# Kernel optimization log

Measured on AMD Instinct MI355X. Metric: run time of the kernel, lower is better.

Reference implementation:

```python
import jax, jax.numpy as jnp
import numpy as np

EPS = 1e-6
SIGMA = 1.0       # get_matrix default sigma
INIT_SIGMA = 1.0  # args.init_sigma


def setup_inputs() -> dict:
    key = jax.random.key(0)
    ks = jax.random.split(key, 12)
    B, T, LD, NB = 16, 2048, 256, 32
    s = 1.0 / np.sqrt(LD)
    E_raw = jax.random.normal(ks[5], (LD, LD), jnp.float32)
    E_w, _ = jnp.linalg.qr(E_raw)  # orthogonal like geotorch.orthogonal
    return {
        "Z": jax.random.normal(ks[0], (B, T, LD), jnp.float32),
        "obs_times": jax.random.uniform(ks[1], (B, T, 1), jnp.float32),
        "D": jax.random.normal(ks[2], (NB, LD), jnp.float32),
        "coeff_W": jax.random.normal(ks[3], (NB, LD), jnp.float32) * s,
        "coeff_b": jnp.zeros((NB,), jnp.float32),
        "E_w": E_w.astype(jnp.float32),
        "B_w": jax.random.normal(ks[6], (LD, LD), jnp.float32) * s,
        "C_w": jax.random.normal(ks[7], (LD, LD), jnp.float32) * s,
        "M_w": jax.random.normal(ks[8], (LD, LD), jnp.float32) * s,
        "init_mean_p": jax.random.normal(ks[9], (LD,), jnp.float32),
        "init_log_var": jax.random.normal(ks[10], (LD,), jnp.float32),
        "y_log_var": jax.random.normal(ks[11], (LD,), jnp.float32),
    }


def _binop(qi, qj):
    # (A_j*A_i, Bu_j + A_j*Bu_i): combine earlier element qi with later qj
    A_i, Bu_i = qi
    A_j, Bu_j = qj
    return (A_j * A_i, Bu_j + A_j * Bu_i)


def reference(Z, obs_times, D, coeff_W, coeff_b, E_w, B_w, C_w, M_w,
              init_mean_p, init_log_var, y_log_var):
    LD = Z.shape[-1]
    # alphas = B(Z)
    alphas = jnp.einsum('btd,ed->bte', Z, B_w)                      # (B,T,LD)
    # get_matrix (vectorized over batch and time)
    A_basis = -(jnp.exp(D) + EPS)                                   # (NB,LD), negative
    A_coeff = jax.nn.softmax(jnp.einsum('btd,nd->btn', alphas, coeff_W) + coeff_b, axis=-1)
    A_mat = jnp.einsum('btn,nd->btd', A_coeff, A_basis)             # (B,T,LD)
    exp_A_m = jnp.exp(A_mat * obs_times)                            # mean transition
    exp_B_m = (exp_A_m - 1.0) / A_mat * alphas
    exp_A_v = jnp.exp(2.0 * A_mat * obs_times)                      # var transition
    exp_B_v = 0.5 * SIGMA ** 2 * (exp_A_v - 1.0) / A_mat + EPS
    mats_A = jnp.concatenate([exp_A_m, exp_A_v], axis=-1)           # (B,T,2LD)
    mats_B = jnp.concatenate([exp_B_m, exp_B_v], axis=-1)           # (B,T,2LD)
    # parallel linear-recurrence scan over time
    cum_A, cum_B = jax.lax.associative_scan(_binop, (mats_A, mats_B), axis=1)
    # initial condition in rotated coordinates
    init_mean0 = E_w.T @ init_mean_p                                # (LD,)
    diag_v = INIT_SIGMA * (jnp.exp(init_log_var) + EPS)
    init_var0 = jnp.einsum('ki,k->i', E_w ** 2, diag_v)             # diag(E^T diag(v) E)
    init_mv = jnp.concatenate([init_mean0, init_var0], axis=0)      # (2LD,)
    imv = cum_A * init_mv                                           # (B,T,2LD)
    init_mean, init_var = imv[..., :LD], imv[..., LD:]
    xs_mean, xs_var = cum_B[..., :LD], cum_B[..., LD:]
    y_var = jnp.exp(y_log_var) + EPS
    # output projections: M(E(.)) and history C(E(Z))
    history = jnp.einsum('btd,ed,fe->btf', Z, E_w, C_w)
    means = jnp.einsum('btd,ed,fe->btf', xs_mean + init_mean, E_w, M_w) + history
    stds = jnp.einsum('btd,ed,fe->btf', jnp.sqrt(xs_var + init_var + y_var), E_w, M_w)
    return means, stds, alphas
```

## Files before the change

kernel.cpp:

```cpp
#include <hip/hip_runtime.h>
#include <math.h>

#define EPS 1e-6f

#define B_   16
#define T_   2048
#define LD   256
#define NB   32
#define BT   (B_ * T_)
#define NCH  64
#define CHUNK (T_ / NCH)

typedef short bf16x8 __attribute__((ext_vector_type(8)));
typedef float f32x4  __attribute__((ext_vector_type(4)));

__device__ __forceinline__ unsigned short f2b(float f) {
    unsigned int u = __float_as_uint(f);
    unsigned int r = (u + 0x7fffu + ((u >> 16) & 1u)) >> 16;
    return (unsigned short)r;
}

__device__ __forceinline__ float b2f(unsigned short h) {
    return __uint_as_float(((unsigned int)h) << 16);
}

__device__ __forceinline__ void gl_lds16(const void* g, void* l) {
    __builtin_amdgcn_global_load_lds(
        (const __attribute__((address_space(1))) unsigned int*)g,
        (__attribute__((address_space(3))) unsigned int*)l, 16, 0, 0);
}

__device__ __forceinline__ void stage_tile(const unsigned short* __restrict__ src,
                                           int row0, int stride, int kb,
                                           unsigned short* lds, int wv, int lane) {
#pragma unroll
    for (int cc = 0; cc < 2; ++cc) {
        int c = wv * 2 + cc;
        int r = c * 16 + (lane >> 2);
        int qd = (lane & 3) ^ ((r >> 1) & 3);
        const unsigned short* g = src + (size_t)(row0 + r) * stride + kb + qd * 8;
        gl_lds16(g, lds + c * 512);
    }
}

__device__ __forceinline__ bf16x8 frag_ld(const unsigned short* lds, int row, int qd) {
    int pq = qd ^ ((row >> 1) & 3);
    return *(const bf16x8*)(lds + row * 32 + pq * 8);
}

__device__ __forceinline__ int u_idx(int i, int d) {
    return ((d >> 5) << 10) + (i << 5) + (((((d >> 3) & 3)) ^ (i & 3)) << 3) + (d & 7);
}

__device__ __forceinline__ void compute_Am(const float* __restrict__ logits,
                                           const float* __restrict__ obs,
                                           const unsigned short* __restrict__ AbTh,
                                           const unsigned short* __restrict__ AbTl,
                                           int bt0,
                                           unsigned int* U,
                                           unsigned short* Ph, unsigned short* Pl,
                                           float* obs_s) {
    int tid = threadIdx.x;
    int l = tid & 31, rg = tid >> 5;
    if (tid < CHUNK) obs_s[tid] = obs[bt0 + tid];
#pragma unroll
    for (int jj = 0; jj < 4; ++jj) {
        int row = rg * 4 + jj;
        float v = logits[(size_t)(bt0 + row) * NB + l];
        float mx = v;
#pragma unroll
        for (int off = 16; off >= 1; off >>= 1) mx = fmaxf(mx, __shfl_xor(mx, off, 32));
        float e = expf(v - mx);
        float s = e;
#pragma unroll
        for (int off = 16; off >= 1; off >>= 1) s += __shfl_xor(s, off, 32);
        float p = e / s;
        unsigned short h = f2b(p);
        int sa = row * 32 + ((((l >> 3) ^ ((row >> 1) & 3))) << 3) + (l & 7);
        Ph[sa] = h;
        Pl[sa] = f2b(p - b2f(h));
    }
    __syncthreads();

    int lane = tid & 63, wv = tid >> 6;
    int qd = lane >> 4, mr = lane & 15;
    bf16x8 ph[2], pl[2];
#pragma unroll
    for (int iT = 0; iT < 2; ++iT) {
        ph[iT] = frag_ld(Ph, iT * 16 + mr, qd);
        pl[iT] = frag_ld(Pl, iT * 16 + mr, qd);
    }
#pragma unroll
    for (int j = 0; j < 4; ++j) {
        int dcol = wv * 64 + j * 16 + mr;
        bf16x8 ah = *(const bf16x8*)(AbTh + dcol * NB + qd * 8);
        bf16x8 al = *(const bf16x8*)(AbTl + dcol * NB + qd * 8);
#pragma unroll
        for (int iT = 0; iT < 2; ++iT) {
            f32x4 acc = (f32x4){0.f, 0.f, 0.f, 0.f};
            acc = __builtin_amdgcn_mfma_f32_16x16x32_bf16(ph[iT], ah, acc, 0, 0, 0);
            acc = __builtin_amdgcn_mfma_f32_16x16x32_bf16(pl[iT], ah, acc, 0, 0, 0);
            acc = __builtin_amdgcn_mfma_f32_16x16x32_bf16(ph[iT], al, acc, 0, 0, 0);
#pragma unroll
            for (int r = 0; r < 4; ++r) {
                int i = iT * 16 + qd * 4 + r;
                U[u_idx(i, dcol)] = __float_as_uint(acc[r]);
            }
        }
    }
    __syncthreads();
}

__global__ __launch_bounds__(256) void k_pre(const float* __restrict__ Z,
                                             const float* __restrict__ Dm,
                                             const float* __restrict__ cw,
                                             const float* __restrict__ Ew,
                                             const float* __restrict__ Bw,
                                             const float* __restrict__ Cw,
                                             const float* __restrict__ Mw,
                                             const float* __restrict__ imp,
                                             const float* __restrict__ ilv,
                                             const float* __restrict__ ylv,
                                             unsigned short* __restrict__ GMh,
                                             unsigned short* __restrict__ GCh,
                                             unsigned short* __restrict__ cwbh,
                                             float* __restrict__ im0,
                                             float* __restrict__ iv0,
                                             float* __restrict__ yv,
                                             unsigned short* __restrict__ AbTh,
                                             unsigned short* __restrict__ AbTl,
                                             unsigned short* __restrict__ Bwh,
                                             unsigned short* __restrict__ Zh) {
    int bid = blockIdx.x;
    int tid = threadIdx.x;
    if (bid < 544) {
        const float* W; const float* E; unsigned short* out; int d0, f0;
        if (bid < 256)      { W = Mw; E = Ew; out = GMh;  d0 = (bid & 15) * 16; f0 = (bid >> 4) * 16; }
        else if (bid < 512) { W = Cw; E = Ew; out = GCh;  d0 = (bid & 15) * 16; f0 = ((bid - 256) >> 4) * 16; }
        else                { W = cw; E = Bw; out = cwbh; d0 = (bid & 15) * 16; f0 = ((bid - 512) >> 4) * 16; }
        __shared__ float Ws[16][17];
        __shared__ float Es[16][17];
        int tx = tid & 15, ty = tid >> 4;
        float acc = 0.f;
        for (int eb = 0; eb < LD; eb += 16) {
            Ws[ty][tx] = W[(f0 + ty) * LD + eb + tx];
            Es[ty][tx] = E[(eb + ty) * LD + d0 + tx];
            __syncthreads();
#pragma unroll
            for (int k = 0; k < 16; ++k) acc = fmaf(Ws[ty][k], Es[k][tx], acc);
            __syncthreads();
        }
        out[(f0 + ty) * LD + d0 + tx] = f2b(acc);
    } else if (bid < 577) {
        int sub = bid - 544;
        int t = tid;
        if (sub == 0) {
            float sm = 0.f, sv = 0.f;
            for (int k = 0; k < LD; ++k) {
                float e = Ew[k * LD + t];
                sm = fmaf(e, imp[k], sm);
                sv = fmaf(e * e, expf(ilv[k]) + EPS, sv);
            }
            im0[t] = sm;
            iv0[t] = sv;
            yv[t]  = expf(ylv[t]) + EPS;
        } else {
            int n = sub - 1;
            float a = -(expf(Dm[n * LD + t]) + EPS);
            unsigned short h = f2b(a);
            AbTh[t * NB + n] = h;
            AbTl[t * NB + n] = f2b(a - b2f(h));
        }
    } else if (bid < 641) {
        int i = (bid - 577) * 256 + tid;
        float4 v = ((const float4*)Bw)[i];
        ((ushort4*)Bwh)[i] = make_ushort4(f2b(v.x), f2b(v.y), f2b(v.z), f2b(v.w));
    } else {
        int i = (bid - 641) * 256 + tid;
        float4 v = ((const float4*)Z)[i];
        ((ushort4*)Zh)[i] = make_ushort4(f2b(v.x), f2b(v.y), f2b(v.z), f2b(v.w));
    }
}

__global__ __launch_bounds__(256) void k_zb(const unsigned short* __restrict__ Zh,
                                            const unsigned short* __restrict__ Bwh,
                                            const unsigned short* __restrict__ cwbh,
                                            const float* __restrict__ cb,
                                            float* __restrict__ alphas,
                                            float* __restrict__ logits) {
    __shared__ unsigned short As[128 * 32];
    __shared__ unsigned short Bs[128 * 32];
    int tid = threadIdx.x, lane = tid & 63, wv = tid >> 6;
    int m0 = blockIdx.x * 128;
    int y  = blockIdx.y;
    if (y < 2) {
        int n0 = y * 128;
        int wm = (wv & 1) * 64, wn = (wv >> 1) * 64;
        f32x4 acc[4][4];
#pragma unroll
        for (int i = 0; i < 4; ++i)
#pragma unroll
            for (int j = 0; j < 4; ++j) acc[i][j] = (f32x4){0.f, 0.f, 0.f, 0.f};
        for (int kb = 0; kb < LD; kb += 32) {
            stage_tile(Zh, m0, LD, kb, As, wv, lane);
            stage_tile(Bwh, n0, LD, kb, Bs, wv, lane);
            __syncthreads();
            int qd = lane >> 4;
            bf16x8 af[4], bf[4];
#pragma unroll
            for (int i = 0; i < 4; ++i) af[i] = frag_ld(As, wm + i * 16 + (lane & 15), qd);
#pragma unroll
            for (int j = 0; j < 4; ++j) bf[j] = frag_ld(Bs, wn + j * 16 + (lane & 15), qd);
#pragma unroll
            for (int i = 0; i < 4; ++i)
#pragma unroll
                for (int j = 0; j < 4; ++j)
                    acc[i][j] = __builtin_amdgcn_mfma_f32_16x16x32_bf16(af[i], bf[j], acc[i][j], 0, 0, 0);
            __syncthreads();
        }
        int col = wn + (lane & 15);
        int rb  = wm + ((lane >> 4) << 2);
#pragma unroll
        for (int i = 0; i < 4; ++i)
#pragma unroll
            for (int j = 0; j < 4; ++j)
#pragma unroll
                for (int r = 0; r < 4; ++r)
                    alphas[(size_t)(m0 + rb + i * 16 + r) * LD + n0 + col + j * 16] = acc[i][j][r];
    } else {
        f32x4 acc[2][2];
#pragma unroll
        for (int i = 0; i < 2; ++i)
#pragma unroll
            for (int j = 0; j < 2; ++j) acc[i][j] = (f32x4){0.f, 0.f, 0.f, 0.f};
        for (int kb = 0; kb < LD; kb += 32) {
            stage_tile(Zh, m0, LD, kb, As, wv, lane);
            if (wv < 2) {
                int r = wv * 16 + (lane >> 2);
                int qd = (lane & 3) ^ ((r >> 1) & 3);
                gl_lds16(cwbh + (size_t)r * LD + kb + qd * 8, Bs + wv * 512);
            }
            __syncthreads();
            int qd = lane >> 4;
            bf16x8 af[2], bff[2];
#pragma unroll
            for (int i = 0; i < 2; ++i) af[i] = frag_ld(As, wv * 32 + i * 16 + (lane & 15), qd);
#pragma unroll
            for (int j = 0; j < 2; ++j) bff[j] = frag_ld(Bs, j * 16 + (lane & 15), qd);
#pragma unroll
            for (int i = 0; i < 2; ++i)
#pragma unroll
                for (int j = 0; j < 2; ++j)
                    acc[i][j] = __builtin_amdgcn_mfma_f32_16x16x32_bf16(af[i], bff[j], acc[i][j], 0, 0, 0);
            __syncthreads();
        }
        int col = lane & 15;
        int rb  = (lane >> 4) << 2;
#pragma unroll
        for (int i = 0; i < 2; ++i)
#pragma unroll
            for (int j = 0; j < 2; ++j)
#pragma unroll
                for (int r = 0; r < 4; ++r) {
                    int row = m0 + wv * 32 + i * 16 + rb + r;
                    int cc  = j * 16 + col;
                    logits[(size_t)row * NB + cc] = acc[i][j][r] + cb[cc];
                }
    }
}

__global__ __launch_bounds__(256) void k_tot(const float* __restrict__ logits,
                                             const float* __restrict__ alphas,
                                             const float* __restrict__ obs,
                                             const unsigned short* __restrict__ AbTh,
                                             const unsigned short* __restrict__ AbTl,
                                             float* __restrict__ totA,
                                             float* __restrict__ totBm,
                                             float* __restrict__ totBv) {
    __shared__ unsigned int U[8192];
    __shared__ unsigned short Ph[1024];
    __shared__ unsigned short Pl[1024];
    __shared__ float obs_s[CHUNK];
    int d = threadIdx.x;
    int bt0 = blockIdx.x * CHUNK;
    compute_Am(logits, obs, AbTh, AbTl, bt0, U, Ph, Pl, obs_s);

    float ra = 1.f, rm = 0.f, rv = 0.f;
    int ubase = ((d >> 5) << 10) + (d & 7);
    int qb = (d >> 3) & 3;
    for (int g = 0; g < 4; ++g) {
        float av[8];
#pragma unroll
        for (int k = 0; k < 8; ++k)
            av[k] = alphas[(size_t)(bt0 + g * 8 + k) * LD + d];
#pragma unroll
        for (int k = 0; k < 8; ++k) {
            int i = g * 8 + k;
            int ui = ubase + (i << 5) + ((qb ^ (i & 3)) << 3);
            float Am = __uint_as_float(U[ui]);
            float eAm = expf(Am * obs_s[i]);
            float ieA = 1.f / Am;
            float eBm = (eAm - 1.f) * ieA * av[k];
            float eBv = 0.5f * (eAm * eAm - 1.f) * ieA + EPS;
            rm = fmaf(eAm, rm, eBm);
            rv = fmaf(eAm * eAm, rv, eBv);
            ra *= eAm;
        }
    }
    int pidx = blockIdx.x * LD + d;
    totA[pidx] = ra; totBm[pidx] = rm; totBv[pidx] = rv;
}

__global__ void k_chunkpfx(const float* __restrict__ totA, const float* __restrict__ totBm,
                           const float* __restrict__ totBv,
                           float* __restrict__ preA, float* __restrict__ preBm,
                           float* __restrict__ preBv) {
    int d = threadIdx.x;
    int b = blockIdx.x;
    float Pa = 1.f, Pm = 0.f, Pv = 0.f;
    for (int ch = 0; ch < NCH; ++ch) {
        int pidx = (b * NCH + ch) * LD + d;
        preA[pidx] = Pa; preBm[pidx] = Pm; preBv[pidx] = Pv;
        float a = totA[pidx], tm_ = totBm[pidx], tv = totBv[pidx];
        Pm = fmaf(a, Pm, tm_);
        Pv = fmaf(a * a, Pv, tv);
        Pa = a * Pa;
    }
}

__global__ __launch_bounds__(256) void k_sms(const float* __restrict__ logits,
                                             const float* __restrict__ alphas,
                                             const float* __restrict__ obs,
                                             const unsigned short* __restrict__ AbTh,
                                             const unsigned short* __restrict__ AbTl,
                                             const float* __restrict__ preA,
                                             const float* __restrict__ preBm,
                                             const float* __restrict__ preBv,
                                             const float* __restrict__ im0,
                                             const float* __restrict__ iv0,
                                             const float* __restrict__ yv,
                                             const unsigned short* __restrict__ Zh,
                                             const unsigned short* __restrict__ GMh,
                                             const unsigned short* __restrict__ GCh,
                                             float* __restrict__ means,
                                             float* __restrict__ stds) {
    __shared__ unsigned int U[8192];
    __shared__ unsigned short Ph[1024];
    __shared__ unsigned short Pl[1024];
    __shared__ float obs_s[CHUNK];
    int tid = threadIdx.x;
    int d = tid;
    int bt0 = blockIdx.x * CHUNK;
    compute_Am(logits, obs, AbTh, AbTl, bt0, U, Ph, Pl, obs_s);

    int pidx = blockIdx.x * LD + d;
    float ga = preA[pidx], gm = preBm[pidx], gv = preBv[pidx];
    float i0 = im0[d], v0 = iv0[d], yvd = yv[d];
    int ubase = ((d >> 5) << 10) + (d & 7);
    int qb = (d >> 3) & 3;
    for (int g = 0; g < 4; ++g) {
        float av[8];
#pragma unroll
        for (int k = 0; k < 8; ++k)
            av[k] = alphas[(size_t)(bt0 + g * 8 + k) * LD + d];
#pragma unroll
        for (int k = 0; k < 8; ++k) {
            int i = g * 8 + k;
            int ui = ubase + (i << 5) + ((qb ^ (i & 3)) << 3);
            float Am = __uint_as_float(U[ui]);
            float eAm = expf(Am * obs_s[i]);
            float ieA = 1.f / Am;
            float eBm = (eAm - 1.f) * ieA * av[k];
            float eBv = 0.5f * (eAm * eAm - 1.f) * ieA + EPS;
            gm = fmaf(eAm, gm, eBm);
            gv = fmaf(eAm * eAm, gv, eBv);
            ga *= eAm;
            float mm = fmaf(ga, i0, gm);
            float vv = fmaf(ga * ga, v0, gv) + yvd;
            U[ui] = ((unsigned int)f2b(mm) << 16) | (unsigned int)f2b(sqrtf(vv));
        }
    }
    __syncthreads();

    int lane = tid & 63, wv = tid >> 6;
    int qd = lane >> 4, mr = lane & 15;
    f32x4 accm[2][4], accs[2][4];
#pragma unroll
    for (int iT = 0; iT < 2; ++iT)
#pragma unroll
        for (int j = 0; j < 4; ++j) {
            accm[iT][j] = (f32x4){0.f, 0.f, 0.f, 0.f};
            accs[iT][j] = (f32x4){0.f, 0.f, 0.f, 0.f};
        }
    for (int kc = 0; kc < 8; ++kc) {
        bf16x8 am[2], asv[2], az[2];
#pragma unroll
        for (int iT = 0; iT < 2; ++iT) {
            int row = iT * 16 + mr;
            int off = (kc << 10) + (row << 5) + ((qd ^ (row & 3)) << 3);
            uint4 ua = *(const uint4*)(U + off);
            uint4 ub = *(const uint4*)(U + off + 4);
            unsigned int uu[8] = {ua.x, ua.y, ua.z, ua.w, ub.x, ub.y, ub.z, ub.w};
            bf16x8 m_, s_;
#pragma unroll
            for (int k = 0; k < 8; ++k) {
                m_[k] = (short)(uu[k] >> 16);
                s_[k] = (short)(uu[k] & 0xffffu);
            }
            am[iT] = m_; asv[iT] = s_;
            az[iT] = *(const bf16x8*)(Zh + (size_t)(bt0 + row) * LD + kc * 32 + qd * 8);
        }
#pragma unroll
        for (int j = 0; j < 4; ++j) {
            int brow = wv * 64 + j * 16 + mr;
            bf16x8 bm = *(const bf16x8*)(GMh + (size_t)brow * LD + kc * 32 + qd * 8);
            bf16x8 bc = *(const bf16x8*)(GCh + (size_t)brow * LD + kc * 32 + qd * 8);
#pragma unroll
            for (int iT = 0; iT < 2; ++iT) {
                accm[iT][j] = __builtin_amdgcn_mfma_f32_16x16x32_bf16(am[iT],  bm, accm[iT][j], 0, 0, 0);
                accs[iT][j] = __builtin_amdgcn_mfma_f32_16x16x32_bf16(asv[iT], bm, accs[iT][j], 0, 0, 0);
                accm[iT][j] = __builtin_amdgcn_mfma_f32_16x16x32_bf16(az[iT],  bc, accm[iT][j], 0, 0, 0);
            }
        }
    }

    int col0 = wv * 64 + mr;
    int rb   = (lane >> 4) << 2;
#pragma unroll
    for (int i = 0; i < 2; ++i)
#pragma unroll
        for (int j = 0; j < 4; ++j)
#pragma unroll
            for (int r = 0; r < 4; ++r) {
                size_t off = (size_t)(bt0 + i * 16 + rb + r) * LD + col0 + j * 16;
                means[off] = accm[i][j][r];
                stds[off]  = accs[i][j][r];
            }
}

extern "C" void kernel_launch(void* const* d_in, const int* in_sizes, int n_in,
                              void* d_out, int out_size, void* d_ws, size_t ws_size,
                              hipStream_t stream) {
    const float* Z   = (const float*)d_in[0];
    const float* obs = (const float*)d_in[1];
    const float* Dm  = (const float*)d_in[2];
    const float* cw  = (const float*)d_in[3];
    const float* cb  = (const float*)d_in[4];
    const float* Ew  = (const float*)d_in[5];
    const float* Bw  = (const float*)d_in[6];
    const float* Cw  = (const float*)d_in[7];
    const float* Mw  = (const float*)d_in[8];
    const float* imp = (const float*)d_in[9];
    const float* ilv = (const float*)d_in[10];
    const float* ylv = (const float*)d_in[11];

    float* out    = (float*)d_out;
    float* means  = out;
    float* stds   = out + (size_t)BT * LD;
    float* alphas = out + (size_t)2 * BT * LD;

    char* ws = (char*)d_ws;
    size_t o = 0;
    unsigned short* Zh   = (unsigned short*)(ws + o); o += (size_t)BT * LD * 2;
    float*          logits=(float*)(ws + o);          o += (size_t)BT * NB * 4;
    unsigned short* GMh  = (unsigned short*)(ws + o); o += (size_t)LD * LD * 2;
    unsigned short* GCh  = (unsigned short*)(ws + o); o += (size_t)LD * LD * 2;
    unsigned short* Bwh  = (unsigned short*)(ws + o); o += (size_t)LD * LD * 2;
    unsigned short* cwbh = (unsigned short*)(ws + o); o += (size_t)NB * LD * 2;
    unsigned short* AbTh = (unsigned short*)(ws + o); o += (size_t)LD * NB * 2;
    unsigned short* AbTl = (unsigned short*)(ws + o); o += (size_t)LD * NB * 2;
    float* totA  = (float*)(ws + o); o += (size_t)B_ * NCH * LD * 4;
    float* totBm = (float*)(ws + o); o += (size_t)B_ * NCH * LD * 4;
    float* totBv = (float*)(ws + o); o += (size_t)B_ * NCH * LD * 4;
    float* preA  = (float*)(ws + o); o += (size_t)B_ * NCH * LD * 4;
    float* preBm = (float*)(ws + o); o += (size_t)B_ * NCH * LD * 4;
    float* preBv = (float*)(ws + o); o += (size_t)B_ * NCH * LD * 4;
    float* im0   = (float*)(ws + o); o += LD * 4;
    float* iv0   = (float*)(ws + o); o += LD * 4;
    float* yv    = (float*)(ws + o); o += LD * 4;

    k_pre<<<dim3(641 + BT * LD / 1024), dim3(256), 0, stream>>>(
        Z, Dm, cw, Ew, Bw, Cw, Mw, imp, ilv, ylv,
        GMh, GCh, cwbh, im0, iv0, yv, AbTh, AbTl, Bwh, Zh);

    k_zb<<<dim3(BT / 128, 3), dim3(256), 0, stream>>>(Zh, Bwh, cwbh, cb, alphas, logits);

    k_tot<<<dim3(B_ * NCH), dim3(256), 0, stream>>>(logits, alphas, obs, AbTh, AbTl,
                                                    totA, totBm, totBv);
    k_chunkpfx<<<dim3(B_), dim3(LD), 0, stream>>>(totA, totBm, totBv, preA, preBm, preBv);

    k_sms<<<dim3(B_ * NCH), dim3(256), 0, stream>>>(logits, alphas, obs, AbTh, AbTl,
                                                    preA, preBm, preBv,
                                                    im0, iv0, yv,
                                                    Zh, GMh, GCh, means, stds);
}
```

Before: 239.7 us.

## Cache softmax bf16 split in logits buffer, prefetch alphas, remap blocks across XCDs

k_tot now writes the split hi/lo bf16 softmax probabilities back into the logits buffer, so k_sms can load the MFMA fragments directly instead of recomputing the softmax. Both kernels load all 32 alphas rows up front, read obs straight from global memory, and use fast exp/rcp intrinsics. Blocks are remapped across XCDs so neighbouring chunks share L2, and k_chunkpfx batches its loads in groups of eight. The fast intrinsics reduce accuracy, and reusing the logits buffer in place couples the two kernels.

```diff
diff --git a/kernel.cpp b/kernel.cpp
--- a/kernel.cpp
+++ b/kernel.cpp
@@ -30,6 +30,11 @@
         (__attribute__((address_space(3))) unsigned int*)l, 16, 0, 0);
 }
 
+__device__ __forceinline__ int xcd_map(int wg) {
+    int x = wg & 7, s = wg >> 3;
+    return (s & 3) | (x << 2) | ((s >> 2) << 5);
+}
+
 __device__ __forceinline__ void stage_tile(const unsigned short* __restrict__ src,
                                            int row0, int stride, int kb,
                                            unsigned short* lds, int wv, int lane) {
@@ -50,65 +55,6 @@
 
 __device__ __forceinline__ int u_idx(int i, int d) {
     return ((d >> 5) << 10) + (i << 5) + (((((d >> 3) & 3)) ^ (i & 3)) << 3) + (d & 7);
-}
-
-__device__ __forceinline__ void compute_Am(const float* __restrict__ logits,
-                                           const float* __restrict__ obs,
-                                           const unsigned short* __restrict__ AbTh,
-                                           const unsigned short* __restrict__ AbTl,
-                                           int bt0,
-                                           unsigned int* U,
-                                           unsigned short* Ph, unsigned short* Pl,
-                                           float* obs_s) {
-    int tid = threadIdx.x;
-    int l = tid & 31, rg = tid >> 5;
-    if (tid < CHUNK) obs_s[tid] = obs[bt0 + tid];
-#pragma unroll
-    for (int jj = 0; jj < 4; ++jj) {
-        int row = rg * 4 + jj;
-        float v = logits[(size_t)(bt0 + row) * NB + l];
-        float mx = v;
-#pragma unroll
-        for (int off = 16; off >= 1; off >>= 1) mx = fmaxf(mx, __shfl_xor(mx, off, 32));
-        float e = expf(v - mx);
-        float s = e;
-#pragma unroll
-        for (int off = 16; off >= 1; off >>= 1) s += __shfl_xor(s, off, 32);
-        float p = e / s;
-        unsigned short h = f2b(p);
-        int sa = row * 32 + ((((l >> 3) ^ ((row >> 1) & 3))) << 3) + (l & 7);
-        Ph[sa] = h;
-        Pl[sa] = f2b(p - b2f(h));
-    }
-    __syncthreads();
-
-    int lane = tid & 63, wv = tid >> 6;
-    int qd = lane >> 4, mr = lane & 15;
-    bf16x8 ph[2], pl[2];
-#pragma unroll
-    for (int iT = 0; iT < 2; ++iT) {
-        ph[iT] = frag_ld(Ph, iT * 16 + mr, qd);
-        pl[iT] = frag_ld(Pl, iT * 16 + mr, qd);
-    }
-#pragma unroll
-    for (int j = 0; j < 4; ++j) {
-        int dcol = wv * 64 + j * 16 + mr;
-        bf16x8 ah = *(const bf16x8*)(AbTh + dcol * NB + qd * 8);
-        bf16x8 al = *(const bf16x8*)(AbTl + dcol * NB + qd * 8);
-#pragma unroll
-        for (int iT = 0; iT < 2; ++iT) {
-            f32x4 acc = (f32x4){0.f, 0.f, 0.f, 0.f};
-            acc = __builtin_amdgcn_mfma_f32_16x16x32_bf16(ph[iT], ah, acc, 0, 0, 0);
-            acc = __builtin_amdgcn_mfma_f32_16x16x32_bf16(pl[iT], ah, acc, 0, 0, 0);
-            acc = __builtin_amdgcn_mfma_f32_16x16x32_bf16(ph[iT], al, acc, 0, 0, 0);
-#pragma unroll
-            for (int r = 0; r < 4; ++r) {
-                int i = iT * 16 + qd * 4 + r;
-                U[u_idx(i, dcol)] = __float_as_uint(acc[r]);
-            }
-        }
-    }
-    __syncthreads();
 }
 
 __global__ __launch_bounds__(256) void k_pre(const float* __restrict__ Z,
@@ -269,7 +215,7 @@
     }
 }
 
-__global__ __launch_bounds__(256) void k_tot(const float* __restrict__ logits,
+__global__ __launch_bounds__(256) void k_tot(float* __restrict__ logits,
                                              const float* __restrict__ alphas,
                                              const float* __restrict__ obs,
                                              const unsigned short* __restrict__ AbTh,
@@ -280,51 +226,109 @@
     __shared__ unsigned int U[8192];
     __shared__ unsigned short Ph[1024];
     __shared__ unsigned short Pl[1024];
-    __shared__ float obs_s[CHUNK];
-    int d = threadIdx.x;
-    int bt0 = blockIdx.x * CHUNK;
-    compute_Am(logits, obs, AbTh, AbTl, bt0, U, Ph, Pl, obs_s);
+    int tid = threadIdx.x;
+    int d = tid;
+    int bid = xcd_map(blockIdx.x);
+    int bt0 = bid * CHUNK;
+
+    float av[32];
+#pragma unroll
+    for (int i = 0; i < 32; ++i) av[i] = alphas[(size_t)(bt0 + i) * LD + d];
+
+    int l = tid & 31, rg = tid >> 5;
+    unsigned int* Pg = (unsigned int*)logits + (size_t)bt0 * NB;
+#pragma unroll
+    for (int jj = 0; jj < 4; ++jj) {
+        int row = rg * 4 + jj;
+        float v = logits[(size_t)(bt0 + row) * NB + l];
+        float mx = v;
+#pragma unroll
+        for (int off = 16; off >= 1; off >>= 1) mx = fmaxf(mx, __shfl_xor(mx, off, 32));
+        float e = __expf(v - mx);
+        float s = e;
+#pragma unroll
+        for (int off = 16; off >= 1; off >>= 1) s += __shfl_xor(s, off, 32);
+        float p = e * __builtin_amdgcn_rcpf(s);
+        unsigned short h = f2b(p);
+        unsigned short lo = f2b(p - b2f(h));
+        int sa = row * 32 + ((((l >> 3) ^ ((row >> 1) & 3))) << 3) + (l & 7);
+        Ph[sa] = h;
+        Pl[sa] = lo;
+        Pg[sa] = ((unsigned int)h << 16) | (unsigned int)lo;
+    }
+    __syncthreads();
+
+    int lane = tid & 63, wv = tid >> 6;
+    int qd = lane >> 4, mr = lane & 15;
+    bf16x8 ph[2], pl[2];
+#pragma unroll
+    for (int iT = 0; iT < 2; ++iT) {
+        ph[iT] = frag_ld(Ph, iT * 16 + mr, qd);
+        pl[iT] = frag_ld(Pl, iT * 16 + mr, qd);
+    }
+#pragma unroll
+    for (int j = 0; j < 4; ++j) {
+        int dcol = wv * 64 + j * 16 + mr;
+        bf16x8 ah = *(const bf16x8*)(AbTh + dcol * NB + qd * 8);
+        bf16x8 al = *(const bf16x8*)(AbTl + dcol * NB + qd * 8);
+#pragma unroll
+        for (int iT = 0; iT < 2; ++iT) {
+            f32x4 acc = (f32x4){0.f, 0.f, 0.f, 0.f};
+            acc = __builtin_amdgcn_mfma_f32_16x16x32_bf16(ph[iT], ah, acc, 0, 0, 0);
+            acc = __builtin_amdgcn_mfma_f32_16x16x32_bf16(pl[iT], ah, acc, 0, 0, 0);
+            acc = __builtin_amdgcn_mfma_f32_16x16x32_bf16(ph[iT], al, acc, 0, 0, 0);
+#pragma unroll
+            for (int r = 0; r < 4; ++r)
+                U[u_idx(iT * 16 + qd * 4 + r, dcol)] = __float_as_uint(acc[r]);
+        }
+    }
+    __syncthreads();
 
     float ra = 1.f, rm = 0.f, rv = 0.f;
     int ubase = ((d >> 5) << 10) + (d & 7);
     int qb = (d >> 3) & 3;
-    for (int g = 0; g < 4; ++g) {
-        float av[8];
-#pragma unroll
-        for (int k = 0; k < 8; ++k)
-            av[k] = alphas[(size_t)(bt0 + g * 8 + k) * LD + d];
-#pragma unroll
-        for (int k = 0; k < 8; ++k) {
-            int i = g * 8 + k;
-            int ui = ubase + (i << 5) + ((qb ^ (i & 3)) << 3);
-            float Am = __uint_as_float(U[ui]);
-            float eAm = expf(Am * obs_s[i]);
-            float ieA = 1.f / Am;
-            float eBm = (eAm - 1.f) * ieA * av[k];
-            float eBv = 0.5f * (eAm * eAm - 1.f) * ieA + EPS;
-            rm = fmaf(eAm, rm, eBm);
-            rv = fmaf(eAm * eAm, rv, eBv);
-            ra *= eAm;
-        }
-    }
-    int pidx = blockIdx.x * LD + d;
+#pragma unroll
+    for (int i = 0; i < CHUNK; ++i) {
+        int ui = ubase + (i << 5) + ((qb ^ (i & 3)) << 3);
+        float Am = __uint_as_float(U[ui]);
+        float tt = obs[bt0 + i];
+        float eAm = __expf(Am * tt);
+        float ieA = __builtin_amdgcn_rcpf(Am);
+        float e2  = eAm * eAm;
+        float eBm = (eAm - 1.f) * ieA * av[i];
+        float eBv = fmaf(0.5f * (e2 - 1.f), ieA, EPS);
+        rm = fmaf(eAm, rm, eBm);
+        rv = fmaf(e2, rv, eBv);
+        ra *= eAm;
+    }
+    int pidx = bid * LD + d;
     totA[pidx] = ra; totBm[pidx] = rm; totBv[pidx] = rv;
 }
 
-__global__ void k_chunkpfx(const float* __restrict__ totA, const float* __restrict__ totBm,
-                           const float* __restrict__ totBv,
-                           float* __restrict__ preA, float* __restrict__ preBm,
-                           float* __restrict__ preBv) {
+__global__ __launch_bounds__(256) void k_chunkpfx(const float* __restrict__ totA,
+                                                  const float* __restrict__ totBm,
+                                                  const float* __restrict__ totBv,
+                                                  float* __restrict__ preA,
+                                                  float* __restrict__ preBm,
+                                                  float* __restrict__ preBv) {
     int d = threadIdx.x;
     int b = blockIdx.x;
     float Pa = 1.f, Pm = 0.f, Pv = 0.f;
-    for (int ch = 0; ch < NCH; ++ch) {
-        int pidx = (b * NCH + ch) * LD + d;
-        preA[pidx] = Pa; preBm[pidx] = Pm; preBv[pidx] = Pv;
-        float a = totA[pidx], tm_ = totBm[pidx], tv = totBv[pidx];
-        Pm = fmaf(a, Pm, tm_);
-        Pv = fmaf(a * a, Pv, tv);
-        Pa = a * Pa;
+    for (int g = 0; g < 8; ++g) {
+        float a8[8], m8[8], v8[8];
+#pragma unroll
+        for (int k = 0; k < 8; ++k) {
+            int pidx = (b * NCH + g * 8 + k) * LD + d;
+            a8[k] = totA[pidx]; m8[k] = totBm[pidx]; v8[k] = totBv[pidx];
+        }
+#pragma unroll
+        for (int k = 0; k < 8; ++k) {
+            int pidx = (b * NCH + g * 8 + k) * LD + d;
+            preA[pidx] = Pa; preBm[pidx] = Pm; preBv[pidx] = Pv;
+            Pm = fmaf(a8[k], Pm, m8[k]);
+            Pv = fmaf(a8[k] * a8[k], Pv, v8[k]);
+            Pa *= a8[k];
+        }
     }
 }
 
@@ -345,45 +349,77 @@
                                              float* __restrict__ means,
                                              float* __restrict__ stds) {
     __shared__ unsigned int U[8192];
-    __shared__ unsigned short Ph[1024];
-    __shared__ unsigned short Pl[1024];
-    __shared__ float obs_s[CHUNK];
-    int tid = threadIdx.x;
+    int tid = threadIdx.x, lane = tid & 63, wv = tid >> 6;
     int d = tid;
-    int bt0 = blockIdx.x * CHUNK;
-    compute_Am(logits, obs, AbTh, AbTl, bt0, U, Ph, Pl, obs_s);
-
-    int pidx = blockIdx.x * LD + d;
+    int bid = xcd_map(blockIdx.x);
+    int bt0 = bid * CHUNK;
+
+    float av[32];
+#pragma unroll
+    for (int i = 0; i < 32; ++i) av[i] = alphas[(size_t)(bt0 + i) * LD + d];
+    int pidx = bid * LD + d;
     float ga = preA[pidx], gm = preBm[pidx], gv = preBv[pidx];
     float i0 = im0[d], v0 = iv0[d], yvd = yv[d];
+
+    int qd = lane >> 4, mr = lane & 15;
+    const unsigned int* Pg = (const unsigned int*)logits + (size_t)bt0 * NB;
+    bf16x8 ph[2], pl[2];
+#pragma unroll
+    for (int iT = 0; iT < 2; ++iT) {
+        int row = iT * 16 + mr;
+        int pq = qd ^ ((row >> 1) & 3);
+        const uint4* q = (const uint4*)(Pg + row * 32 + pq * 8);
+        uint4 wa = q[0], wb = q[1];
+        unsigned int w[8] = {wa.x, wa.y, wa.z, wa.w, wb.x, wb.y, wb.z, wb.w};
+        bf16x8 hh, ll;
+#pragma unroll
+        for (int k = 0; k < 8; ++k) {
+            hh[k] = (short)(w[k] >> 16);
+            ll[k] = (short)(w[k] & 0xffffu);
+        }
+        ph[iT] = hh; pl[iT] = ll;
+    }
+
+#pragma unroll
+    for (int j = 0; j < 4; ++j) {
+        int dcol = wv * 64 + j * 16 + mr;
+        bf16x8 ah = *(const bf16x8*)(AbTh + dcol * NB + qd * 8);
+        bf16x8 al = *(const bf16x8*)(AbTl + dcol * NB + qd * 8);
+#pragma unroll
+        for (int iT = 0; iT < 2; ++iT) {
+            f32x4 acc = (f32x4){0.f, 0.f, 0.f, 0.f};
+            acc = __builtin_amdgcn_mfma_f32_16x16x32_bf16(ph[iT], ah, acc, 0, 0, 0);
+            acc = __builtin_amdgcn_mfma_f32_16x16x32_bf16(pl[iT], ah, acc, 0, 0, 0);
+            acc = __builtin_amdgcn_mfma_f32_16x16x32_bf16(ph[iT], al, acc, 0, 0, 0);
+#pragma unroll
+            for (int r = 0; r < 4; ++r)
+                U[u_idx(iT * 16 + qd * 4 + r, dcol)] = __float_as_uint(acc[r]);
+        }
+    }
+    __syncthreads();
+
     int ubase = ((d >> 5) << 10) + (d & 7);
     int qb = (d >> 3) & 3;
-    for (int g = 0; g < 4; ++g) {
-        float av[8];
-#pragma unroll
-        for (int k = 0; k < 8; ++k)
-            av[k] = alphas[(size_t)(bt0 + g * 8 + k) * LD + d];
-#pragma unroll
-        for (int k = 0; k < 8; ++k) {
-            int i = g * 8 + k;
-            int ui = ubase + (i << 5) + ((qb ^ (i & 3)) << 3);
-            float Am = __uint_as_float(U[ui]);
-            float eAm = expf(Am * obs_s[i]);
-            float ieA = 1.f / Am;
-            float eBm = (eAm - 1.f) * ieA * av[k];
-            float eBv = 0.5f * (eAm * eAm - 1.f) * ieA + EPS;
-            gm = fmaf(eAm, gm, eBm);
-            gv = fmaf(eAm * eAm, gv, eBv);
-            ga *= eAm;
-            float mm = fmaf(ga, i0, gm);
-            float vv = fmaf(ga * ga, v0, gv) + yvd;
-            U[ui] = ((unsigned int)f2b(mm) << 16) | (unsigned int)f2b(sqrtf(vv));
-        }
+#pragma unroll
+    for (int i = 0; i < CHUNK; ++i) {
+        int ui = ubase + (i << 5) + ((qb ^ (i & 3)) << 3);
+        float Am = __uint_as_float(U[ui]);
+        float tt = obs[bt0 + i];
+        float eAm = __expf(Am * tt);
+        float ieA = __builtin_amdgcn_rcpf(Am);
+        float e2  = eAm * eAm;
+        float eBm = (eAm - 1.f) * ieA * av[i];
+        float eBv = fmaf(0.5f * (e2 - 1.f), ieA, EPS);
+        gm = fmaf(eAm, gm, eBm);
+        gv = fmaf(e2, gv, eBv);
+        ga *= eAm;
+        float mm = fmaf(ga, i0, gm);
+        float vv = fmaf(ga * ga, v0, gv) + yvd;
+        float ss = sqrtf(vv);
+        U[ui] = ((unsigned int)f2b(mm) << 16) | (unsigned int)f2b(ss);
     }
     __syncthreads();
 
-    int lane = tid & 63, wv = tid >> 6;
-    int qd = lane >> 4, mr = lane & 15;
     f32x4 accm[2][4], accs[2][4];
 #pragma unroll
     for (int iT = 0; iT < 2; ++iT)
```

Result: no change. 237.0 us (-1.1%).
